# Kernel optimization log

Measured on AMD Instinct MI355X. Metric: run time of the kernel, lower is better.

Reference implementation:

```python
import jax, jax.numpy as jnp
import numpy as np

HIDDEN = 128
N_H = 32
E = 262144


def setup_inputs() -> dict:
    key = jax.random.key(0)
    ks = jax.random.split(key, 10)
    s = lambda fan_in: 1.0 / np.sqrt(fan_in)
    return {
        "h_i": jax.random.normal(ks[0], (E, N_H), dtype=jnp.float32),
        "e_ij": jax.random.normal(ks[1], (E, 1), dtype=jnp.float32),
        # lin_A1: 1 -> HIDDEN
        "W_A1": jax.random.uniform(ks[2], (1, HIDDEN), jnp.float32, -s(1), s(1)),
        "b_A1": jnp.zeros((HIDDEN,), jnp.float32),
        # lin_A2: HIDDEN -> N_H*N_H
        "W_A2": jax.random.uniform(ks[3], (HIDDEN, N_H * N_H), jnp.float32, -s(HIDDEN), s(HIDDEN)),
        "b_A2": jnp.zeros((N_H * N_H,), jnp.float32),
        # lin_b1: 1 -> HIDDEN
        "W_b1": jax.random.uniform(ks[4], (1, HIDDEN), jnp.float32, -s(1), s(1)),
        "b_b1": jnp.zeros((HIDDEN,), jnp.float32),
        # lin_b2: HIDDEN -> N_H
        "W_b2": jax.random.uniform(ks[5], (HIDDEN, N_H), jnp.float32, -s(HIDDEN), s(HIDDEN)),
        "b_b2": jnp.zeros((N_H,), jnp.float32),
    }


def reference(h_i, e_ij, W_A1, b_A1, W_A2, b_A2, W_b1, b_b1, W_b2, b_b2):
    # Per-edge MLP producing an [N_H, N_H] matrix A from the scalar edge feature
    A = jax.nn.selu(e_ij @ W_A1 + b_A1)          # [E, HIDDEN]
    A = (A @ W_A2 + b_A2).reshape(-1, N_H, N_H)  # [E, N_H, N_H]
    # Per-edge MLP producing an [N_H] bias b
    b = jax.nn.selu(e_ij @ W_b1 + b_b1)          # [E, HIDDEN]
    b = b @ W_b2 + b_b2                          # [E, N_H]
    # Batched matvec: m_ij[e, i] = sum_j A[e, i, j] * h_i[e, j] + b[e, i]
    m_ij = jnp.einsum('eij,ej->ei', A, h_i) + b
    return m_ij
```

## Files before the change

### kernel.cpp

```cpp
#include <hip/hip_runtime.h>

#define NH       32
#define HID      128
#define E_TOT    262144
#define CH_ELEM  8192
#define NCH_MAIN 16
#define NCH_ALL  17

typedef float        f32x4 __attribute__((ext_vector_type(4)));
typedef short        s16x8 __attribute__((ext_vector_type(8)));
typedef unsigned int u32x4 __attribute__((ext_vector_type(4)));

static __device__ __forceinline__ short f2bf(float f) {
    __bf16 b = (__bf16)f;
    return __builtin_bit_cast(short, b);
}
static __device__ __forceinline__ float selu_f(float x) {
    const float kScale  = 1.0507009873554804934193349852946f;
    const float kAlphaS = 1.7580993408473768599402175208123f;
    float neg = kAlphaS * (__expf(x) - 1.0f);
    return x > 0.0f ? kScale * x : neg;
}

__global__ void wt_build(const float* __restrict__ W_A2, const float* __restrict__ b_A2,
                         const float* __restrict__ W_b2, unsigned short* __restrict__ WT) {
    int gid = blockIdx.x * 256 + threadIdx.x;
    if (gid >= NCH_ALL * CH_ELEM) return;
    int c    = gid >> 13;
    int r    = gid & 8191;
    int sl   = r >> 10;
    int it   = (r >> 9) & 1;
    int g    = (r >> 7) & 3;
    int lrow = (r >> 3) & 15;
    int p    = r & 7;
    int i    = it * 16 + lrow;
    int kap  = c * 256 + sl * 32 + g * 8 + p;
    float v = 0.0f;
    if (kap < 4096)      v = W_A2[(kap >> 5) * 1024 + i * 32 + (kap & 31)];
    else if (kap < 4128) v = b_A2[i * 32 + (kap - 4096)];
    else if (kap < 4256) v = W_b2[(kap - 4128) * 32 + i];
    WT[gid] = (unsigned short)f2bf(v);
}

typedef const __attribute__((address_space(1))) unsigned int GU32;
typedef __attribute__((address_space(3))) unsigned int LU32;
static __device__ __forceinline__ void gload_lds16(const void* g, void* l) {
    __builtin_amdgcn_global_load_lds((GU32*)g, (LU32*)l, 16, 0, 0);
}

__global__ void __launch_bounds__(256, 3)
msg_main(const float* __restrict__ h_i, const float* __restrict__ e_ij,
         const float* __restrict__ W_A1, const float* __restrict__ b_A1,
         const float* __restrict__ W_b1, const float* __restrict__ b_b1,
         const float* __restrict__ b_b2,
         const unsigned short* __restrict__ WT,
         float* __restrict__ out)
{
    __shared__ unsigned short ldsW[2][CH_ELEM];
    __shared__ float cA1[HID], cBA1[HID], cB1a[HID], cB1b[HID], cb2[NH];

    const int tid  = threadIdx.x;
    const int lane = tid & 63;
    const int wid  = tid >> 6;
    const int lrow = lane & 15;
    const int g    = lane >> 4;
    const int e0   = blockIdx.x * 256 + wid * 64;

    if (tid < HID) {
        cA1[tid]  = W_A1[tid];
        cBA1[tid] = b_A1[tid];
        cB1a[tid] = W_b1[tid];
        cB1b[tid] = b_b1[tid];
    }
    if (tid < NH) cb2[tid] = b_b2[tid];

    const float ev_own = e_ij[e0 + lane];

    s16x8 hb[4];
    #pragma unroll
    for (int ct = 0; ct < 4; ++ct) {
        int er = e0 + ct * 16 + lrow;
        const float* hp = h_i + er * 32 + g * 8;
        f32x4 h0 = *(const f32x4*)hp;
        f32x4 h1 = *(const f32x4*)(hp + 4);
        #pragma unroll
        for (int p = 0; p < 4; ++p) {
            hb[ct][p]     = f2bf(h0[p]);
            hb[ct][p + 4] = f2bf(h1[p]);
        }
    }

    float ev_ct[4];
    #pragma unroll
    for (int ct = 0; ct < 4; ++ct) ev_ct[ct] = __shfl(ev_own, ct * 16 + lrow);

    f32x4 acc[4][2];
    #pragma unroll
    for (int ct = 0; ct < 4; ++ct)
        #pragma unroll
        for (int it = 0; it < 2; ++it)
            acc[ct][it] = (f32x4){0.f, 0.f, 0.f, 0.f};
    const f32x4 zf = (f32x4){0.f, 0.f, 0.f, 0.f};

    float u_own[8];

    auto stage = [&](int b, int c) {
        #pragma unroll
        for (int r = 0; r < 4; ++r) {
            int eo = wid * 2048 + r * 512;
            gload_lds16(WT + c * CH_ELEM + eo + lane * 8, &ldsW[b][eo]);
        }
    };
    auto ufill = [&](int c) {
        #pragma unroll
        for (int sl = 0; sl < 8; ++sl) {
            int s = c * 8 + sl;
            u_own[sl] = selu_f(fmaf(ev_own, cA1[s], cBA1[s]));
        }
    };

    __syncthreads();
    stage(0, 0);
    ufill(0);
    __syncthreads();

    int buf = 0;
    for (int c = 0; c < NCH_MAIN; ++c) {
        stage(buf ^ 1, c + 1);
        #pragma unroll
        for (int sl = 0; sl < 8; ++sl) {
            u32x4 r0 = *(const u32x4*)&ldsW[buf][sl * 1024 +       lane * 8];
            u32x4 r1 = *(const u32x4*)&ldsW[buf][sl * 1024 + 512 + lane * 8];
            s16x8 A0 = __builtin_bit_cast(s16x8, r0);
            s16x8 A1 = __builtin_bit_cast(s16x8, r1);
            #pragma unroll
            for (int ct = 0; ct < 4; ++ct) {
                float uv = __shfl(u_own[sl], ct * 16 + lrow);
                f32x4 t0 = __builtin_amdgcn_mfma_f32_16x16x32_bf16(A0, hb[ct], zf, 0, 0, 0);
                f32x4 t1 = __builtin_amdgcn_mfma_f32_16x16x32_bf16(A1, hb[ct], zf, 0, 0, 0);
                f32x4 u4 = (f32x4){uv, uv, uv, uv};
                acc[ct][0] = __builtin_elementwise_fma(t0, u4, acc[ct][0]);
                acc[ct][1] = __builtin_elementwise_fma(t1, u4, acc[ct][1]);
            }
        }
        if (c + 1 < NCH_MAIN) ufill(c + 1);
        __syncthreads();
        buf ^= 1;
    }

    {
        u32x4 r0 = *(const u32x4*)&ldsW[buf][      lane * 8];
        u32x4 r1 = *(const u32x4*)&ldsW[buf][512 + lane * 8];
        s16x8 A0 = __builtin_bit_cast(s16x8, r0);
        s16x8 A1 = __builtin_bit_cast(s16x8, r1);
        #pragma unroll
        for (int ct = 0; ct < 4; ++ct) {
            acc[ct][0] = __builtin_amdgcn_mfma_f32_16x16x32_bf16(A0, hb[ct], acc[ct][0], 0, 0, 0);
            acc[ct][1] = __builtin_amdgcn_mfma_f32_16x16x32_bf16(A1, hb[ct], acc[ct][1], 0, 0, 0);
        }
    }
    #pragma unroll
    for (int q = 0; q < 4; ++q) {
        u32x4 r0 = *(const u32x4*)&ldsW[buf][(q + 1) * 1024 +       lane * 8];
        u32x4 r1 = *(const u32x4*)&ldsW[buf][(q + 1) * 1024 + 512 + lane * 8];
        s16x8 A0 = __builtin_bit_cast(s16x8, r0);
        s16x8 A1 = __builtin_bit_cast(s16x8, r1);
        int tb = q * 32 + g * 8;
        f32x4 wb0 = *(const f32x4*)&cB1a[tb];
        f32x4 wb1 = *(const f32x4*)&cB1a[tb + 4];
        f32x4 bb0 = *(const f32x4*)&cB1b[tb];
        f32x4 bb1 = *(const f32x4*)&cB1b[tb + 4];
        #pragma unroll
        for (int ct = 0; ct < 4; ++ct) {
            s16x8 B;
            #pragma unroll
            for (int p = 0; p < 4; ++p) {
                B[p]     = f2bf(selu_f(fmaf(ev_ct[ct], wb0[p], bb0[p])));
                B[p + 4] = f2bf(selu_f(fmaf(ev_ct[ct], wb1[p], bb1[p])));
            }
            acc[ct][0] = __builtin_amdgcn_mfma_f32_16x16x32_bf16(A0, B, acc[ct][0], 0, 0, 0);
            acc[ct][1] = __builtin_amdgcn_mfma_f32_16x16x32_bf16(A1, B, acc[ct][1], 0, 0, 0);
        }
    }

    #pragma unroll
    for (int it = 0; it < 2; ++it) {
        f32x4 b2v = *(const f32x4*)&cb2[it * 16 + g * 4];
        #pragma unroll
        for (int ct = 0; ct < 4; ++ct) {
            int edge = e0 + ct * 16 + lrow;
            f32x4 vo = acc[ct][it] + b2v;
            *(f32x4*)&out[edge * 32 + it * 16 + g * 4] = vo;
        }
    }
}

extern "C" void kernel_launch(void* const* d_in, const int* in_sizes, int n_in,
                              void* d_out, int out_size, void* d_ws, size_t ws_size,
                              hipStream_t stream) {
    const float* h_i  = (const float*)d_in[0];
    const float* e_ij = (const float*)d_in[1];
    const float* W_A1 = (const float*)d_in[2];
    const float* b_A1 = (const float*)d_in[3];
    const float* W_A2 = (const float*)d_in[4];
    const float* b_A2 = (const float*)d_in[5];
    const float* W_b1 = (const float*)d_in[6];
    const float* b_b1 = (const float*)d_in[7];
    const float* W_b2 = (const float*)d_in[8];
    const float* b_b2 = (const float*)d_in[9];

    unsigned short* WT = (unsigned short*)d_ws;

    wt_build<<<(NCH_ALL * CH_ELEM + 255) / 256, 256, 0, stream>>>(W_A2, b_A2, W_b2, WT);
    msg_main<<<E_TOT / 256, 256, 0, stream>>>(h_i, e_ij, W_A1, b_A1, W_b1, b_b1,
                                              b_b2, WT, (float*)d_out);
}
```

Measured before the change: 110.9 us.

## Replace double-buffered weight staging with single larger LDS chunk and higher occupancy

Weight chunks grow from 256 to 512 K-rows, held in one 32 KB LDS buffer instead of two 16 KB buffers, and are loaded synchronously before each compute phase rather than prefetched. The tail (bias and W_b2 rows) is split out into its own small region. Launch bounds rise to 4 blocks per CU, with the MFMA/FMA issue order regrouped into batches of four. The aim is to hide load latency through more resident waves and fewer barriers instead of in-block double buffering. The risk is exposed global-to-LDS latency at each chunk boundary and register pressure from the 4-block bound.

```diff
diff --git a/kernel.cpp b/kernel.cpp
--- a/kernel.cpp
+++ b/kernel.cpp
@@ -1,11 +1,12 @@
 #include <hip/hip_runtime.h>
 
-#define NH       32
-#define HID      128
-#define E_TOT    262144
-#define CH_ELEM  8192
-#define NCH_MAIN 16
-#define NCH_ALL  17
+#define NH        32
+#define HID       128
+#define E_TOT     262144
+#define CH_ELEM   16384
+#define NCH_MAIN  8
+#define TAIL_OFF  131072
+#define TAIL_ELEM 8192
 
 typedef float        f32x4 __attribute__((ext_vector_type(4)));
 typedef short        s16x8 __attribute__((ext_vector_type(8)));
@@ -25,16 +26,27 @@
 __global__ void wt_build(const float* __restrict__ W_A2, const float* __restrict__ b_A2,
                          const float* __restrict__ W_b2, unsigned short* __restrict__ WT) {
     int gid = blockIdx.x * 256 + threadIdx.x;
-    if (gid >= NCH_ALL * CH_ELEM) return;
-    int c    = gid >> 13;
-    int r    = gid & 8191;
-    int sl   = r >> 10;
-    int it   = (r >> 9) & 1;
-    int g    = (r >> 7) & 3;
-    int lrow = (r >> 3) & 15;
-    int p    = r & 7;
-    int i    = it * 16 + lrow;
-    int kap  = c * 256 + sl * 32 + g * 8 + p;
+    if (gid >= TAIL_OFF + TAIL_ELEM) return;
+    int it, g, lrow, p, kap;
+    if (gid < TAIL_OFF) {
+        int c  = gid >> 14;
+        int r  = gid & 16383;
+        int sl = r >> 10;
+        it   = (r >> 9) & 1;
+        g    = (r >> 7) & 3;
+        lrow = (r >> 3) & 15;
+        p    = r & 7;
+        kap  = c * 512 + sl * 32 + g * 8 + p;
+    } else {
+        int r  = gid - TAIL_OFF;
+        int sl = r >> 10;
+        it   = (r >> 9) & 1;
+        g    = (r >> 7) & 3;
+        lrow = (r >> 3) & 15;
+        p    = r & 7;
+        kap  = 4096 + sl * 32 + g * 8 + p;
+    }
+    int i = it * 16 + lrow;
     float v = 0.0f;
     if (kap < 4096)      v = W_A2[(kap >> 5) * 1024 + i * 32 + (kap & 31)];
     else if (kap < 4128) v = b_A2[i * 32 + (kap - 4096)];
@@ -48,7 +60,7 @@
     __builtin_amdgcn_global_load_lds((GU32*)g, (LU32*)l, 16, 0, 0);
 }
 
-__global__ void __launch_bounds__(256, 3)
+__global__ void __launch_bounds__(256, 4)
 msg_main(const float* __restrict__ h_i, const float* __restrict__ e_ij,
          const float* __restrict__ W_A1, const float* __restrict__ b_A1,
          const float* __restrict__ W_b1, const float* __restrict__ b_b1,
@@ -56,7 +68,7 @@
          const unsigned short* __restrict__ WT,
          float* __restrict__ out)
 {
-    __shared__ unsigned short ldsW[2][CH_ELEM];
+    __shared__ unsigned short ldsW[CH_ELEM];
     __shared__ float cA1[HID], cBA1[HID], cB1a[HID], cB1b[HID], cb2[NH];
 
     const int tid  = threadIdx.x;
@@ -102,55 +114,67 @@
             acc[ct][it] = (f32x4){0.f, 0.f, 0.f, 0.f};
     const f32x4 zf = (f32x4){0.f, 0.f, 0.f, 0.f};
 
-    float u_own[8];
-
-    auto stage = [&](int b, int c) {
-        #pragma unroll
-        for (int r = 0; r < 4; ++r) {
-            int eo = wid * 2048 + r * 512;
-            gload_lds16(WT + c * CH_ELEM + eo + lane * 8, &ldsW[b][eo]);
-        }
-    };
-    auto ufill = [&](int c) {
-        #pragma unroll
-        for (int sl = 0; sl < 8; ++sl) {
-            int s = c * 8 + sl;
+    float u_own[16];
+
+    __syncthreads();
+
+    for (int c = 0; c < NCH_MAIN; ++c) {
+        #pragma unroll
+        for (int r = 0; r < 8; ++r) {
+            int eo = r * 2048 + tid * 8;
+            gload_lds16(WT + c * CH_ELEM + eo, &ldsW[eo]);
+        }
+        #pragma unroll
+        for (int sl = 0; sl < 16; ++sl) {
+            int s = c * 16 + sl;
             u_own[sl] = selu_f(fmaf(ev_own, cA1[s], cBA1[s]));
         }
-    };
-
-    __syncthreads();
-    stage(0, 0);
-    ufill(0);
-    __syncthreads();
-
-    int buf = 0;
-    for (int c = 0; c < NCH_MAIN; ++c) {
-        stage(buf ^ 1, c + 1);
-        #pragma unroll
-        for (int sl = 0; sl < 8; ++sl) {
-            u32x4 r0 = *(const u32x4*)&ldsW[buf][sl * 1024 +       lane * 8];
-            u32x4 r1 = *(const u32x4*)&ldsW[buf][sl * 1024 + 512 + lane * 8];
+        __syncthreads();
+
+        #pragma unroll
+        for (int sl = 0; sl < 16; ++sl) {
+            u32x4 r0 = *(const u32x4*)&ldsW[sl * 1024 +       lane * 8];
+            u32x4 r1 = *(const u32x4*)&ldsW[sl * 1024 + 512 + lane * 8];
             s16x8 A0 = __builtin_bit_cast(s16x8, r0);
             s16x8 A1 = __builtin_bit_cast(s16x8, r1);
+            f32x4 u4[4];
             #pragma unroll
             for (int ct = 0; ct < 4; ++ct) {
                 float uv = __shfl(u_own[sl], ct * 16 + lrow);
-                f32x4 t0 = __builtin_amdgcn_mfma_f32_16x16x32_bf16(A0, hb[ct], zf, 0, 0, 0);
-                f32x4 t1 = __builtin_amdgcn_mfma_f32_16x16x32_bf16(A1, hb[ct], zf, 0, 0, 0);
-                f32x4 u4 = (f32x4){uv, uv, uv, uv};
-                acc[ct][0] = __builtin_elementwise_fma(t0, u4, acc[ct][0]);
-                acc[ct][1] = __builtin_elementwise_fma(t1, u4, acc[ct][1]);
-            }
-        }
-        if (c + 1 < NCH_MAIN) ufill(c + 1);
+                u4[ct] = (f32x4){uv, uv, uv, uv};
+            }
+            {
+                f32x4 t[4];
+                #pragma unroll
+                for (int ct = 0; ct < 4; ++ct)
+                    t[ct] = __builtin_amdgcn_mfma_f32_16x16x32_bf16(A0, hb[ct], zf, 0, 0, 0);
+                #pragma unroll
+                for (int ct = 0; ct < 4; ++ct)
+                    acc[ct][0] = __builtin_elementwise_fma(t[ct], u4[ct], acc[ct][0]);
+            }
+            {
+                f32x4 t[4];
+                #pragma unroll
+                for (int ct = 0; ct < 4; ++ct)
+                    t[ct] = __builtin_amdgcn_mfma_f32_16x16x32_bf16(A1, hb[ct], zf, 0, 0, 0);
+                #pragma unroll
+                for (int ct = 0; ct < 4; ++ct)
+                    acc[ct][1] = __builtin_elementwise_fma(t[ct], u4[ct], acc[ct][1]);
+            }
+        }
         __syncthreads();
-        buf ^= 1;
-    }
+    }
+
+    #pragma unroll
+    for (int r = 0; r < 3; ++r) {
+        int eo = r * 2048 + tid * 8;
+        gload_lds16(WT + TAIL_OFF + eo, &ldsW[eo]);
+    }
+    __syncthreads();
 
     {
-        u32x4 r0 = *(const u32x4*)&ldsW[buf][      lane * 8];
-        u32x4 r1 = *(const u32x4*)&ldsW[buf][512 + lane * 8];
+        u32x4 r0 = *(const u32x4*)&ldsW[      lane * 8];
+        u32x4 r1 = *(const u32x4*)&ldsW[512 + lane * 8];
         s16x8 A0 = __builtin_bit_cast(s16x8, r0);
         s16x8 A1 = __builtin_bit_cast(s16x8, r1);
         #pragma unroll
@@ -161,8 +185,8 @@
     }
     #pragma unroll
     for (int q = 0; q < 4; ++q) {
-        u32x4 r0 = *(const u32x4*)&ldsW[buf][(q + 1) * 1024 +       lane * 8];
-        u32x4 r1 = *(const u32x4*)&ldsW[buf][(q + 1) * 1024 + 512 + lane * 8];
+        u32x4 r0 = *(const u32x4*)&ldsW[(q + 1) * 1024 +       lane * 8];
+        u32x4 r1 = *(const u32x4*)&ldsW[(q + 1) * 1024 + 512 + lane * 8];
         s16x8 A0 = __builtin_bit_cast(s16x8, r0);
         s16x8 A1 = __builtin_bit_cast(s16x8, r1);
         int tb = q * 32 + g * 8;
@@ -211,7 +235,7 @@
 
     unsigned short* WT = (unsigned short*)d_ws;
 
-    wt_build<<<(NCH_ALL * CH_ELEM + 255) / 256, 256, 0, stream>>>(W_A2, b_A2, W_b2, WT);
+    wt_build<<<(TAIL_OFF + TAIL_ELEM + 255) / 256, 256, 0, stream>>>(W_A2, b_A2, W_b2, WT);
     msg_main<<<E_TOT / 256, 256, 0, stream>>>(h_i, e_ij, W_A1, b_A1, W_b1, b_b1,
                                               b_b2, WT, (float*)d_out);
 }
```

After: 97.62 us. -11.9%, faster.
